# Optimization experiments

Hardware: AMD Instinct MI355X
Metric: run time of the kernel (lower is better)

The kernel has to match this reference:

```python
import jax, jax.numpy as jnp
import numpy as np

N, E, F, H, B = 100000, 3200000, 128, 32, 256
NEG_SLOPE = 0.2  # PyG GATv2Conv default negative_slope


def setup_inputs() -> dict:
    key = jax.random.key(0)
    ks = jax.random.split(key, 8)
    x = jax.random.normal(ks[0], (N, F), jnp.float32)
    edge_index = jax.random.randint(ks[1], (2, E), 0, N, dtype=jnp.int32)
    # sorted graph ids covering all B graphs (PyG batch vector is sorted)
    batch = (jnp.arange(N, dtype=jnp.int32) * B) // N
    init = lambda k, shape, fan: (jax.random.normal(k, shape, jnp.float32) / np.float32(np.sqrt(fan)))
    Wl = init(ks[2], (F, H), F)
    Wr = init(ks[3], (F, H), F)
    att = init(ks[4], (H,), H)
    bias = jnp.zeros((H,), jnp.float32)
    W1 = init(ks[5], (H, 1024), H); b1 = jnp.zeros((1024,), jnp.float32)
    W2 = init(ks[6], (1024, 512), 1024); b2 = jnp.zeros((512,), jnp.float32)
    W3 = init(ks[7], (512, 4), 512); b3 = jnp.zeros((4,), jnp.float32)
    return dict(x=x, edge_index=edge_index, batch=batch, Wl=Wl, Wr=Wr,
                att=att, bias=bias, W1=W1, b1=b1, W2=W2, b2=b2, W3=W3, b3=b3)


def reference(x, edge_index, batch, Wl, Wr, att, bias, W1, b1, W2, b2, W3, b3):
    # ---- GATv2Conv (single head, sum aggregation, self-loops added) ----
    loop = jnp.arange(N, dtype=edge_index.dtype)
    src = jnp.concatenate([edge_index[0], loop])  # [E+N] message sources
    dst = jnp.concatenate([edge_index[1], loop])  # [E+N] message targets
    xl = x @ Wl  # [N,H] source-side transform
    xr = x @ Wr  # [N,H] target-side transform
    # GATv2 score: a^T LeakyReLU(Wl x_src + Wr x_dst)
    e = jax.nn.leaky_relu(xl[src] + xr[dst], NEG_SLOPE) @ att  # [E+N]
    # segment softmax over incoming edges of each target node
    m = jax.ops.segment_max(e, dst, num_segments=N)  # every node has a self-loop
    p = jnp.exp(e - m[dst])
    z = jax.ops.segment_sum(p, dst, num_segments=N)
    alpha = p / z[dst]  # [E+N]
    node_out = jax.ops.segment_sum(alpha[:, None] * xl[src], dst, num_segments=N) + bias  # [N,H]
    # ---- global max pool over each graph ----
    g = jax.ops.segment_max(node_out, batch, num_segments=B)  # [B,H]
    # ---- classification MLP head ----
    h = jax.nn.relu(g @ W1 + b1)
    h = jax.nn.relu(h @ W2 + b2)
    return h @ W3 + b3  # [B,4]
```

## Files before the change

### kernel.cpp

```cpp
#include <hip/hip_runtime.h>
#include <hip/hip_fp16.h>

#define N_NODES 100000
#define N_EDGES 3200000
#define F_IN    128
#define H_DIM   32
#define B_GR    256
#define NEG     0.2f

#define FBIN_SZ  125
#define N_FBIN   (N_NODES / FBIN_SZ)
#define BIN_CAP  5120
#define CPAD     16
#define PART_T   1024
#define EPB_R    8
#define EPB_G    (PART_T * EPB_R)
#define PART_NBLK ((N_EDGES / 4 + EPB_G - 1) / EPB_G)
#define LIN_BLK  ((N_NODES + 63) / 64)

__device__ __forceinline__ unsigned fenc(float f) {
    unsigned u = __float_as_uint(f);
    return (u & 0x80000000u) ? ~u : (u | 0x80000000u);
}
__device__ __forceinline__ float fdec(unsigned u) {
    return (u & 0x80000000u) ? __uint_as_float(u & 0x7FFFFFFFu)
                             : __uint_as_float(~u);
}

__global__ __launch_bounds__(1024) void k_fused(
    const int* __restrict__ ei, int* __restrict__ bcnt, unsigned* __restrict__ binbuf,
    const float* __restrict__ x, const float* __restrict__ Wl,
    const float* __restrict__ Wr, __half* __restrict__ xl16, float* __restrict__ xr)
{
    __shared__ __align__(16) float smem[16384];
    int t = threadIdx.x;

    if (blockIdx.x < PART_NBLK) {
        int* lcnt = (int*)smem;
        int* cur  = lcnt + 1024;
        lcnt[t] = 0;
        __syncthreads();
        int g0 = blockIdx.x * EPB_G;
        const int4* dsrc = (const int4*)(ei + N_EDGES);
        const int4* ssrc = (const int4*)ei;
        #pragma unroll
        for (int r = 0; r < EPB_R; ++r) {
            int i = g0 + r * PART_T + t;
            if (i < N_EDGES / 4) {
                int4 d = dsrc[i];
                atomicAdd(&lcnt[d.x / FBIN_SZ], 1);
                atomicAdd(&lcnt[d.y / FBIN_SZ], 1);
                atomicAdd(&lcnt[d.z / FBIN_SZ], 1);
                atomicAdd(&lcnt[d.w / FBIN_SZ], 1);
            }
        }
        __syncthreads();
        if (t < N_FBIN) {
            int c = lcnt[t];
            if (c > 0) cur[t] = atomicAdd(&bcnt[t * CPAD], c);
        }
        __syncthreads();
        #pragma unroll
        for (int r = 0; r < EPB_R; ++r) {
            int i = g0 + r * PART_T + t;
            if (i < N_EDGES / 4) {
                int4 s = ssrc[i];
                int4 d = dsrc[i];
                int b, p;
                b = d.x / FBIN_SZ; p = atomicAdd(&cur[b], 1);
                binbuf[(size_t)b * BIN_CAP + p] = ((unsigned)(d.x - b * FBIN_SZ) << 17) | (unsigned)s.x;
                b = d.y / FBIN_SZ; p = atomicAdd(&cur[b], 1);
                binbuf[(size_t)b * BIN_CAP + p] = ((unsigned)(d.y - b * FBIN_SZ) << 17) | (unsigned)s.y;
                b = d.z / FBIN_SZ; p = atomicAdd(&cur[b], 1);
                binbuf[(size_t)b * BIN_CAP + p] = ((unsigned)(d.z - b * FBIN_SZ) << 17) | (unsigned)s.z;
                b = d.w / FBIN_SZ; p = atomicAdd(&cur[b], 1);
                binbuf[(size_t)b * BIN_CAP + p] = ((unsigned)(d.w - b * FBIN_SZ) << 17) | (unsigned)s.w;
            }
        }
    } else {
        float* Wls = smem;
        float* Wrs = smem + 4096;
        float* xsb = smem + 8192;
        int blk = blockIdx.x - PART_NBLK;
        for (int i = t; i < F_IN * H_DIM; i += 1024) { Wls[i] = Wl[i]; Wrs[i] = Wr[i]; }
        int q = t >> 8, tq = t & 255;
        size_t base = (size_t)blk * 64 + q * 16;
        bool act = base < N_NODES;
        float* xs = xsb + q * 2048;
        if (act) {
            const float4* xg = (const float4*)(x + base * F_IN);
            float4* xs4 = (float4*)xs;
            xs4[tq] = xg[tq];
            xs4[tq + 256] = xg[tq + 256];
        }
        __syncthreads();
        if (act) {
            int nl = tq >> 5, h = tq & 31;
            float al0 = 0.f, ar0 = 0.f, al1 = 0.f, ar1 = 0.f;
            const float4* xa4 = (const float4*)(xs + nl * F_IN);
            const float4* xb4 = (const float4*)(xs + (nl + 8) * F_IN);
            #pragma unroll 8
            for (int f4 = 0; f4 < 32; ++f4) {
                float4 xa = xa4[f4], xb = xb4[f4];
                int fb = f4 * 4;
                float w;
                w = Wls[(fb + 0) * 32 + h]; al0 = fmaf(xa.x, w, al0); al1 = fmaf(xb.x, w, al1);
                w = Wls[(fb + 1) * 32 + h]; al0 = fmaf(xa.y, w, al0); al1 = fmaf(xb.y, w, al1);
                w = Wls[(fb + 2) * 32 + h]; al0 = fmaf(xa.z, w, al0); al1 = fmaf(xb.z, w, al1);
                w = Wls[(fb + 3) * 32 + h]; al0 = fmaf(xa.w, w, al0); al1 = fmaf(xb.w, w, al1);
                w = Wrs[(fb + 0) * 32 + h]; ar0 = fmaf(xa.x, w, ar0); ar1 = fmaf(xb.x, w, ar1);
                w = Wrs[(fb + 1) * 32 + h]; ar0 = fmaf(xa.y, w, ar0); ar1 = fmaf(xb.y, w, ar1);
                w = Wrs[(fb + 2) * 32 + h]; ar0 = fmaf(xa.z, w, ar0); ar1 = fmaf(xb.z, w, ar1);
                w = Wrs[(fb + 3) * 32 + h]; ar0 = fmaf(xa.w, w, ar0); ar1 = fmaf(xb.w, w, ar1);
            }
            size_t n0 = base + nl, n1 = base + nl + 8;
            xl16[n0 * 32 + h] = __float2half(al0); xr[n0 * 32 + h] = ar0;
            xl16[n1 * 32 + h] = __float2half(al1); xr[n1 * 32 + h] = ar1;
        }
    }
}

__global__ __launch_bounds__(512) void k_aggregate(
    const unsigned* __restrict__ binbuf, const int* __restrict__ bcnt,
    const __half* __restrict__ xl16, const float* __restrict__ xr,
    const float* __restrict__ att, const float* __restrict__ bias,
    const int* __restrict__ batch, unsigned* __restrict__ gu)
{
    __shared__ unsigned eL[BIN_CAP];
    __shared__ int cnt[128];
    __shared__ int sc[128];
    __shared__ int cur[128];
    __shared__ unsigned lmax[64];
    int t = threadIdx.x;
    int bin = blockIdx.x;
    int n_e = bcnt[bin * CPAD];
    const unsigned* bb = binbuf + (size_t)bin * BIN_CAP;

    if (t < 128) cnt[t] = 0;
    if (t < 64) lmax[t] = 0u;
    __syncthreads();
    for (int i = t; i < n_e; i += 512)
        atomicAdd(&cnt[bb[i] >> 17], 1);
    __syncthreads();
    if (t < 128) sc[t] = cnt[t];
    __syncthreads();
    for (int off = 1; off < 128; off <<= 1) {
        int v = 0;
        if (t < 128 && t >= off) v = sc[t - off];
        __syncthreads();
        if (t < 128) sc[t] += v;
        __syncthreads();
    }
    if (t < 128) cur[t] = sc[t] - cnt[t];
    __syncthreads();
    for (int i = t; i < n_e; i += 512) {
        unsigned u = bb[i];
        int p = atomicAdd(&cur[u >> 17], 1);
        eL[p] = u;
    }
    __syncthreads();

    int lane = t & 63;
    int wv = t >> 6;
    int ns = (lane >> 4) & 3;
    int stream = (lane >> 3) & 1;
    int oct = lane & 7;
    const float4 a4 = ((const float4*)att)[oct];
    const float4 b4 = ((const float4*)bias)[oct];
    int lg0 = batch[bin * FBIN_SZ];

    for (int nl = wv * 4 + ns; nl < FBIN_SZ; nl += 32) {
        int n = bin * FBIN_SZ + nl;
        int e0 = (nl > 0) ? sc[nl - 1] : 0;
        int e1 = sc[nl];
        const float4 xr4 = ((const float4*)(xr + (size_t)n * H_DIM))[oct];
        float2 raw = ((const float2*)(xl16 + (size_t)n * H_DIM))[oct];
        float2 sf0 = __half22float2(*(__half2*)&raw.x);
        float2 sf1 = __half22float2(*(__half2*)&raw.y);

        float z = 0.f;
        float4 acc = make_float4(0.f, 0.f, 0.f, 0.f);
        {
            float vx = sf0.x + xr4.x; vx = fmaxf(vx, vx * NEG);
            float vy = sf0.y + xr4.y; vy = fmaxf(vy, vy * NEG);
            float vz = sf1.x + xr4.z; vz = fmaxf(vz, vz * NEG);
            float vw = sf1.y + xr4.w; vw = fmaxf(vw, vw * NEG);
            float pr = vx * a4.x;
            pr = fmaf(vy, a4.y, pr);
            pr = fmaf(vz, a4.z, pr);
            pr = fmaf(vw, a4.w, pr);
            pr += __shfl_xor(pr, 1);
            pr += __shfl_xor(pr, 2);
            pr += __shfl_xor(pr, 4);
            if (stream == 0) {
                float p = __expf(fminf(pr, 70.f));
                z = p;
                acc = make_float4(p * sf0.x, p * sf0.y, p * sf1.x, p * sf1.y);
            }
        }

        int j = e0 + stream;
        for (; j + 2 < e1; j += 4) {
            unsigned uA = eL[j], uB = eL[j + 2];
            int sA = (int)(uA & 0x1FFFFu), sB = (int)(uB & 0x1FFFFu);
            float2 rA = ((const float2*)(xl16 + (size_t)sA * H_DIM))[oct];
            float2 rB = ((const float2*)(xl16 + (size_t)sB * H_DIM))[oct];
            float2 A0 = __half22float2(*(__half2*)&rA.x);
            float2 A1 = __half22float2(*(__half2*)&rA.y);
            float2 B0 = __half22float2(*(__half2*)&rB.x);
            float2 B1 = __half22float2(*(__half2*)&rB.y);
            float pA, pB;
            {
                float vx = A0.x + xr4.x; vx = fmaxf(vx, vx * NEG);
                float vy = A0.y + xr4.y; vy = fmaxf(vy, vy * NEG);
                float vz = A1.x + xr4.z; vz = fmaxf(vz, vz * NEG);
                float vw = A1.y + xr4.w; vw = fmaxf(vw, vw * NEG);
                pA = vx * a4.x; pA = fmaf(vy, a4.y, pA);
                pA = fmaf(vz, a4.z, pA); pA = fmaf(vw, a4.w, pA);
            }
            {
                float vx = B0.x + xr4.x; vx = fmaxf(vx, vx * NEG);
                float vy = B0.y + xr4.y; vy = fmaxf(vy, vy * NEG);
                float vz = B1.x + xr4.z; vz = fmaxf(vz, vz * NEG);
                float vw = B1.y + xr4.w; vw = fmaxf(vw, vw * NEG);
                pB = vx * a4.x; pB = fmaf(vy, a4.y, pB);
                pB = fmaf(vz, a4.z, pB); pB = fmaf(vw, a4.w, pB);
            }
            pA += __shfl_xor(pA, 1); pB += __shfl_xor(pB, 1);
            pA += __shfl_xor(pA, 2); pB += __shfl_xor(pB, 2);
            pA += __shfl_xor(pA, 4); pB += __shfl_xor(pB, 4);
            float eA = __expf(fminf(pA, 70.f));
            float eB = __expf(fminf(pB, 70.f));
            z += eA + eB;
            acc.x = fmaf(eA, A0.x, acc.x); acc.y = fmaf(eA, A0.y, acc.y);
            acc.z = fmaf(eA, A1.x, acc.z); acc.w = fmaf(eA, A1.y, acc.w);
            acc.x = fmaf(eB, B0.x, acc.x); acc.y = fmaf(eB, B0.y, acc.y);
            acc.z = fmaf(eB, B1.x, acc.z); acc.w = fmaf(eB, B1.y, acc.w);
        }
        for (; j < e1; j += 2) {
            unsigned u = eL[j];
            int s = (int)(u & 0x1FFFFu);
            float2 rS = ((const float2*)(xl16 + (size_t)s * H_DIM))[oct];
            float2 S0 = __half22float2(*(__half2*)&rS.x);
            float2 S1 = __half22float2(*(__half2*)&rS.y);
            float vx = S0.x + xr4.x; vx = fmaxf(vx, vx * NEG);
            float vy = S0.y + xr4.y; vy = fmaxf(vy, vy * NEG);
            float vz = S1.x + xr4.z; vz = fmaxf(vz, vz * NEG);
            float vw = S1.y + xr4.w; vw = fmaxf(vw, vw * NEG);
            float pp = vx * a4.x; pp = fmaf(vy, a4.y, pp);
            pp = fmaf(vz, a4.z, pp); pp = fmaf(vw, a4.w, pp);
            pp += __shfl_xor(pp, 1);
            pp += __shfl_xor(pp, 2);
            pp += __shfl_xor(pp, 4);
            float p = __expf(fminf(pp, 70.f));
            z += p;
            acc.x = fmaf(p, S0.x, acc.x); acc.y = fmaf(p, S0.y, acc.y);
            acc.z = fmaf(p, S1.x, acc.z); acc.w = fmaf(p, S1.y, acc.w);
        }

        z += __shfl_xor(z, 8);
        acc.x += __shfl_xor(acc.x, 8);
        acc.y += __shfl_xor(acc.y, 8);
        acc.z += __shfl_xor(acc.z, 8);
        acc.w += __shfl_xor(acc.w, 8);

        if (stream == 0) {
            float inv = 1.f / z;
            int gi = batch[n] - lg0;
            int base = gi * 32 + oct * 4;
            atomicMax(&lmax[base + 0], fenc(fmaf(acc.x, inv, b4.x)));
            atomicMax(&lmax[base + 1], fenc(fmaf(acc.y, inv, b4.y)));
            atomicMax(&lmax[base + 2], fenc(fmaf(acc.z, inv, b4.z)));
            atomicMax(&lmax[base + 3], fenc(fmaf(acc.w, inv, b4.w)));
        }
    }
    __syncthreads();
    if (t < 64) {
        int g = lg0 + (t >> 5);
        int glast = batch[bin * FBIN_SZ + FBIN_SZ - 1];
        if (g <= glast) atomicMax(&gu[g * H_DIM + (t & 31)], lmax[t]);
    }
}

__global__ __launch_bounds__(512) void k_head(
    const unsigned* __restrict__ gu, const float* __restrict__ W1,
    const float* __restrict__ b1, const float* __restrict__ W2,
    const float* __restrict__ b2, const float* __restrict__ W3,
    const float* __restrict__ b3, float* __restrict__ out)
{
    __shared__ float gs[H_DIM];
    __shared__ float h1s[1024];
    __shared__ float h2s[512];
    int b = blockIdx.x, t = threadIdx.x;
    if (t < H_DIM) gs[t] = fdec(gu[b * H_DIM + t]);
    __syncthreads();
    #pragma unroll
    for (int jj = 0; jj < 2; ++jj) {
        int j = jj * 512 + t;
        float a = b1[j];
        #pragma unroll
        for (int k = 0; k < H_DIM; ++k) a = fmaf(gs[k], W1[k * 1024 + j], a);
        h1s[j] = fmaxf(a, 0.f);
    }
    __syncthreads();
    {
        float a0 = 0.f, a1 = 0.f, a2 = 0.f, a3 = 0.f;
        #pragma unroll 4
        for (int k = 0; k < 256; ++k) {
            a0 = fmaf(h1s[k      ], W2[(size_t)(k      ) * 512 + t], a0);
            a1 = fmaf(h1s[k + 256], W2[(size_t)(k + 256) * 512 + t], a1);
            a2 = fmaf(h1s[k + 512], W2[(size_t)(k + 512) * 512 + t], a2);
            a3 = fmaf(h1s[k + 768], W2[(size_t)(k + 768) * 512 + t], a3);
        }
        h2s[t] = fmaxf((a0 + a1) + (a2 + a3) + b2[t], 0.f);
    }
    __syncthreads();
    if (t < 256) {
        int c = t >> 6, lane = t & 63;
        float a = 0.f;
        #pragma unroll
        for (int k = lane; k < 512; k += 64)
            a = fmaf(h2s[k], W3[k * 4 + c], a);
        for (int off = 32; off; off >>= 1) a += __shfl_down(a, off);
        if (lane == 0) out[b * 4 + c] = a + b3[c];
    }
}

extern "C" void kernel_launch(void* const* d_in, const int* in_sizes, int n_in,
                              void* d_out, int out_size, void* d_ws, size_t ws_size,
                              hipStream_t stream)
{
    const float* x     = (const float*)d_in[0];
    const int*   ei    = (const int*)d_in[1];
    const int*   batch = (const int*)d_in[2];
    const float* Wl    = (const float*)d_in[3];
    const float* Wr    = (const float*)d_in[4];
    const float* att   = (const float*)d_in[5];
    const float* bias  = (const float*)d_in[6];
    const float* W1    = (const float*)d_in[7];
    const float* b1    = (const float*)d_in[8];
    const float* W2    = (const float*)d_in[9];
    const float* b2    = (const float*)d_in[10];
    const float* W3    = (const float*)d_in[11];
    const float* b3    = (const float*)d_in[12];
    float* out = (float*)d_out;

    __half*   xl16   = (__half*)d_ws;
    float*    xr     = (float*)(xl16 + (size_t)N_NODES * H_DIM);
    unsigned* binbuf = (unsigned*)(xr + (size_t)N_NODES * H_DIM);
    int*      bcnt   = (int*)(binbuf + (size_t)N_FBIN * BIN_CAP);
    unsigned* gu     = (unsigned*)(bcnt + N_FBIN * CPAD);

    hipMemsetAsync(bcnt, 0, (size_t)(N_FBIN * CPAD + B_GR * H_DIM) * sizeof(int), stream);

    k_fused<<<PART_NBLK + LIN_BLK, 1024, 0, stream>>>(
        ei, bcnt, binbuf, x, Wl, Wr, xl16, xr);
    k_aggregate<<<N_FBIN, 512, 0, stream>>>(binbuf, bcnt, xl16, xr, att, bias, batch, gu);
    k_head<<<B_GR, 512, 0, stream>>>(gu, W1, b1, W2, b2, W3, b3, out);
}
```

Measured before the change: 156.5 us.

## Replace global bin atomics with per-block segmented partition and store xr in fp16

Each partition block now computes a local exclusive scan of its per-bin counts and writes its edges contiguously into its own region, recording per-block segment offsets. This replaces the global atomicAdd on bin counters and the scattered writes into fixed-capacity bins. The aggregate kernel then gathers each bin's edges from all partition blocks' segments, which fragments its reads into many short runs. Separately, xr is stored as fp16 to halve that buffer's traffic, at some cost in precision.

```diff
diff --git a/kernel.cpp b/kernel.cpp
--- a/kernel.cpp
+++ b/kernel.cpp
@@ -11,11 +11,12 @@
 #define FBIN_SZ  125
 #define N_FBIN   (N_NODES / FBIN_SZ)
 #define BIN_CAP  5120
-#define CPAD     16
 #define PART_T   1024
 #define EPB_R    8
 #define EPB_G    (PART_T * EPB_R)
-#define PART_NBLK ((N_EDGES / 4 + EPB_G - 1) / EPB_G)
+#define EPB_E    (EPB_G * 4)
+#define PART_NBLK ((N_EDGES + EPB_E - 1) / EPB_E)
+#define SEG_STRIDE (N_FBIN + 1)
 #define LIN_BLK  ((N_NODES + 63) / 64)
 
 __device__ __forceinline__ unsigned fenc(float f) {
@@ -28,9 +29,9 @@
 }
 
 __global__ __launch_bounds__(1024) void k_fused(
-    const int* __restrict__ ei, int* __restrict__ bcnt, unsigned* __restrict__ binbuf,
+    const int* __restrict__ ei, int* __restrict__ segofs, unsigned* __restrict__ binbuf,
     const float* __restrict__ x, const float* __restrict__ Wl,
-    const float* __restrict__ Wr, __half* __restrict__ xl16, float* __restrict__ xr)
+    const float* __restrict__ Wr, __half* __restrict__ xl16, __half* __restrict__ xr16)
 {
     __shared__ __align__(16) float smem[16384];
     int t = threadIdx.x;
@@ -38,9 +39,11 @@
     if (blockIdx.x < PART_NBLK) {
         int* lcnt = (int*)smem;
         int* cur  = lcnt + 1024;
+        int* wsum = cur + 1024;
+        int blk = blockIdx.x;
         lcnt[t] = 0;
         __syncthreads();
-        int g0 = blockIdx.x * EPB_G;
+        int g0 = blk * EPB_G;
         const int4* dsrc = (const int4*)(ei + N_EDGES);
         const int4* ssrc = (const int4*)ei;
         #pragma unroll
@@ -55,11 +58,27 @@
             }
         }
         __syncthreads();
-        if (t < N_FBIN) {
-            int c = lcnt[t];
-            if (c > 0) cur[t] = atomicAdd(&bcnt[t * CPAD], c);
-        }
-        __syncthreads();
+        int lane = t & 63, w = t >> 6;
+        int v = lcnt[t];
+        int inc = v;
+        #pragma unroll
+        for (int off = 1; off < 64; off <<= 1) {
+            int u2 = __shfl_up(inc, off);
+            if (lane >= off) inc += u2;
+        }
+        if (lane == 63) wsum[w] = inc;
+        __syncthreads();
+        if (t == 0) {
+            int run = 0;
+            #pragma unroll
+            for (int k = 0; k < 16; ++k) { int vv = wsum[k]; wsum[k] = run; run += vv; }
+        }
+        __syncthreads();
+        int excl = inc - v + wsum[w];
+        cur[t] = excl;
+        if (t <= N_FBIN) segofs[(size_t)blk * SEG_STRIDE + t] = excl;
+        __syncthreads();
+        size_t blkbase = (size_t)blk * EPB_E;
         #pragma unroll
         for (int r = 0; r < EPB_R; ++r) {
             int i = g0 + r * PART_T + t;
@@ -68,13 +87,13 @@
                 int4 d = dsrc[i];
                 int b, p;
                 b = d.x / FBIN_SZ; p = atomicAdd(&cur[b], 1);
-                binbuf[(size_t)b * BIN_CAP + p] = ((unsigned)(d.x - b * FBIN_SZ) << 17) | (unsigned)s.x;
+                binbuf[blkbase + p] = ((unsigned)(d.x - b * FBIN_SZ) << 17) | (unsigned)s.x;
                 b = d.y / FBIN_SZ; p = atomicAdd(&cur[b], 1);
-                binbuf[(size_t)b * BIN_CAP + p] = ((unsigned)(d.y - b * FBIN_SZ) << 17) | (unsigned)s.y;
+                binbuf[blkbase + p] = ((unsigned)(d.y - b * FBIN_SZ) << 17) | (unsigned)s.y;
                 b = d.z / FBIN_SZ; p = atomicAdd(&cur[b], 1);
-                binbuf[(size_t)b * BIN_CAP + p] = ((unsigned)(d.z - b * FBIN_SZ) << 17) | (unsigned)s.z;
+                binbuf[blkbase + p] = ((unsigned)(d.z - b * FBIN_SZ) << 17) | (unsigned)s.z;
                 b = d.w / FBIN_SZ; p = atomicAdd(&cur[b], 1);
-                binbuf[(size_t)b * BIN_CAP + p] = ((unsigned)(d.w - b * FBIN_SZ) << 17) | (unsigned)s.w;
+                binbuf[blkbase + p] = ((unsigned)(d.w - b * FBIN_SZ) << 17) | (unsigned)s.w;
             }
         }
     } else {
@@ -114,15 +133,15 @@
                 w = Wrs[(fb + 3) * 32 + h]; ar0 = fmaf(xa.w, w, ar0); ar1 = fmaf(xb.w, w, ar1);
             }
             size_t n0 = base + nl, n1 = base + nl + 8;
-            xl16[n0 * 32 + h] = __float2half(al0); xr[n0 * 32 + h] = ar0;
-            xl16[n1 * 32 + h] = __float2half(al1); xr[n1 * 32 + h] = ar1;
+            xl16[n0 * 32 + h] = __float2half(al0); xr16[n0 * 32 + h] = __float2half(ar0);
+            xl16[n1 * 32 + h] = __float2half(al1); xr16[n1 * 32 + h] = __float2half(ar1);
         }
     }
 }
 
 __global__ __launch_bounds__(512) void k_aggregate(
-    const unsigned* __restrict__ binbuf, const int* __restrict__ bcnt,
-    const __half* __restrict__ xl16, const float* __restrict__ xr,
+    const unsigned* __restrict__ binbuf, const int* __restrict__ segofs,
+    const __half* __restrict__ xl16, const __half* __restrict__ xr16,
     const float* __restrict__ att, const float* __restrict__ bias,
     const int* __restrict__ batch, unsigned* __restrict__ gu)
 {
@@ -130,17 +149,27 @@
     __shared__ int cnt[128];
     __shared__ int sc[128];
     __shared__ int cur[128];
+    __shared__ int llen[PART_NBLK];
+    __shared__ int sbase[PART_NBLK];
     __shared__ unsigned lmax[64];
     int t = threadIdx.x;
     int bin = blockIdx.x;
-    int n_e = bcnt[bin * CPAD];
-    const unsigned* bb = binbuf + (size_t)bin * BIN_CAP;
-
+    int lane = t & 63;
+    int wv = t >> 6;
+
+    if (t < PART_NBLK) {
+        int a = segofs[(size_t)t * SEG_STRIDE + bin];
+        llen[t]  = segofs[(size_t)t * SEG_STRIDE + bin + 1] - a;
+        sbase[t] = t * EPB_E + a;
+    }
     if (t < 128) cnt[t] = 0;
     if (t < 64) lmax[t] = 0u;
     __syncthreads();
-    for (int i = t; i < n_e; i += 512)
-        atomicAdd(&cnt[bb[i] >> 17], 1);
+    for (int k = wv; k < PART_NBLK; k += 8) {
+        int gb = sbase[k], L = llen[k];
+        for (int i = lane; i < L; i += 64)
+            atomicAdd(&cnt[binbuf[gb + i] >> 17], 1);
+    }
     __syncthreads();
     if (t < 128) sc[t] = cnt[t];
     __syncthreads();
@@ -153,15 +182,16 @@
     }
     if (t < 128) cur[t] = sc[t] - cnt[t];
     __syncthreads();
-    for (int i = t; i < n_e; i += 512) {
-        unsigned u = bb[i];
-        int p = atomicAdd(&cur[u >> 17], 1);
-        eL[p] = u;
-    }
-    __syncthreads();
-
-    int lane = t & 63;
-    int wv = t >> 6;
+    for (int k = wv; k < PART_NBLK; k += 8) {
+        int gb = sbase[k], L = llen[k];
+        for (int i = lane; i < L; i += 64) {
+            unsigned u = binbuf[gb + i];
+            int p = atomicAdd(&cur[u >> 17], 1);
+            eL[p] = u;
+        }
+    }
+    __syncthreads();
+
     int ns = (lane >> 4) & 3;
     int stream = (lane >> 3) & 1;
     int oct = lane & 7;
@@ -173,7 +203,9 @@
         int n = bin * FBIN_SZ + nl;
         int e0 = (nl > 0) ? sc[nl - 1] : 0;
         int e1 = sc[nl];
-        const float4 xr4 = ((const float4*)(xr + (size_t)n * H_DIM))[oct];
+        float2 rawr = ((const float2*)(xr16 + (size_t)n * H_DIM))[oct];
+        float2 xr0 = __half22float2(*(__half2*)&rawr.x);
+        float2 xr1 = __half22float2(*(__half2*)&rawr.y);
         float2 raw = ((const float2*)(xl16 + (size_t)n * H_DIM))[oct];
         float2 sf0 = __half22float2(*(__half2*)&raw.x);
         float2 sf1 = __half22float2(*(__half2*)&raw.y);
@@ -181,10 +213,10 @@
         float z = 0.f;
         float4 acc = make_float4(0.f, 0.f, 0.f, 0.f);
         {
-            float vx = sf0.x + xr4.x; vx = fmaxf(vx, vx * NEG);
-            float vy = sf0.y + xr4.y; vy = fmaxf(vy, vy * NEG);
-            float vz = sf1.x + xr4.z; vz = fmaxf(vz, vz * NEG);
-            float vw = sf1.y + xr4.w; vw = fmaxf(vw, vw * NEG);
+            float vx = sf0.x + xr0.x; vx = fmaxf(vx, vx * NEG);
+            float vy = sf0.y + xr0.y; vy = fmaxf(vy, vy * NEG);
+            float vz = sf1.x + xr1.x; vz = fmaxf(vz, vz * NEG);
+            float vw = sf1.y + xr1.y; vw = fmaxf(vw, vw * NEG);
             float pr = vx * a4.x;
             pr = fmaf(vy, a4.y, pr);
             pr = fmaf(vz, a4.z, pr);
@@ -211,18 +243,18 @@
             float2 B1 = __half22float2(*(__half2*)&rB.y);
             float pA, pB;
             {
-                float vx = A0.x + xr4.x; vx = fmaxf(vx, vx * NEG);
-                float vy = A0.y + xr4.y; vy = fmaxf(vy, vy * NEG);
-                float vz = A1.x + xr4.z; vz = fmaxf(vz, vz * NEG);
-                float vw = A1.y + xr4.w; vw = fmaxf(vw, vw * NEG);
+                float vx = A0.x + xr0.x; vx = fmaxf(vx, vx * NEG);
+                float vy = A0.y + xr0.y; vy = fmaxf(vy, vy * NEG);
+                float vz = A1.x + xr1.x; vz = fmaxf(vz, vz * NEG);
+                float vw = A1.y + xr1.y; vw = fmaxf(vw, vw * NEG);
                 pA = vx * a4.x; pA = fmaf(vy, a4.y, pA);
                 pA = fmaf(vz, a4.z, pA); pA = fmaf(vw, a4.w, pA);
             }
             {
-                float vx = B0.x + xr4.x; vx = fmaxf(vx, vx * NEG);
-                float vy = B0.y + xr4.y; vy = fmaxf(vy, vy * NEG);
-                float vz = B1.x + xr4.z; vz = fmaxf(vz, vz * NEG);
-                float vw = B1.y + xr4.w; vw = fmaxf(vw, vw * NEG);
+                float vx = B0.x + xr0.x; vx = fmaxf(vx, vx * NEG);
+                float vy = B0.y + xr0.y; vy = fmaxf(vy, vy * NEG);
+                float vz = B1.x + xr1.x; vz = fmaxf(vz, vz * NEG);
+                float vw = B1.y + xr1.y; vw = fmaxf(vw, vw * NEG);
                 pB = vx * a4.x; pB = fmaf(vy, a4.y, pB);
                 pB = fmaf(vz, a4.z, pB); pB = fmaf(vw, a4.w, pB);
             }
@@ -243,10 +275,10 @@
             float2 rS = ((const float2*)(xl16 + (size_t)s * H_DIM))[oct];
             float2 S0 = __half22float2(*(__half2*)&rS.x);
             float2 S1 = __half22float2(*(__half2*)&rS.y);
-            float vx = S0.x + xr4.x; vx = fmaxf(vx, vx * NEG);
-            float vy = S0.y + xr4.y; vy = fmaxf(vy, vy * NEG);
-            float vz = S1.x + xr4.z; vz = fmaxf(vz, vz * NEG);
-            float vw = S1.y + xr4.w; vw = fmaxf(vw, vw * NEG);
+            float vx = S0.x + xr0.x; vx = fmaxf(vx, vx * NEG);
+            float vy = S0.y + xr0.y; vy = fmaxf(vy, vy * NEG);
+            float vz = S1.x + xr1.x; vz = fmaxf(vz, vz * NEG);
+            float vw = S1.y + xr1.y; vw = fmaxf(vw, vw * NEG);
             float pp = vx * a4.x; pp = fmaf(vy, a4.y, pp);
             pp = fmaf(vz, a4.z, pp); pp = fmaf(vw, a4.w, pp);
             pp += __shfl_xor(pp, 1);
@@ -346,15 +378,15 @@
     float* out = (float*)d_out;
 
     __half*   xl16   = (__half*)d_ws;
-    float*    xr     = (float*)(xl16 + (size_t)N_NODES * H_DIM);
-    unsigned* binbuf = (unsigned*)(xr + (size_t)N_NODES * H_DIM);
-    int*      bcnt   = (int*)(binbuf + (size_t)N_FBIN * BIN_CAP);
-    unsigned* gu     = (unsigned*)(bcnt + N_FBIN * CPAD);
-
-    hipMemsetAsync(bcnt, 0, (size_t)(N_FBIN * CPAD + B_GR * H_DIM) * sizeof(int), stream);
+    __half*   xr16   = xl16 + (size_t)N_NODES * H_DIM;
+    unsigned* binbuf = (unsigned*)(xr16 + (size_t)N_NODES * H_DIM);
+    int*      segofs = (int*)(binbuf + (size_t)PART_NBLK * EPB_E);
+    unsigned* gu     = (unsigned*)(segofs + (size_t)PART_NBLK * SEG_STRIDE);
+
+    hipMemsetAsync(gu, 0, (size_t)B_GR * H_DIM * sizeof(int), stream);
 
     k_fused<<<PART_NBLK + LIN_BLK, 1024, 0, stream>>>(
-        ei, bcnt, binbuf, x, Wl, Wr, xl16, xr);
-    k_aggregate<<<N_FBIN, 512, 0, stream>>>(binbuf, bcnt, xl16, xr, att, bias, batch, gu);
+        ei, segofs, binbuf, x, Wl, Wr, xl16, xr16);
+    k_aggregate<<<N_FBIN, 512, 0, stream>>>(binbuf, segofs, xl16, xr16, att, bias, batch, gu);
     k_head<<<B_GR, 512, 0, stream>>>(gu, W1, b1, W2, b2, W3, b3, out);
 }
```

Result: slower. 165.2 us (+5.5%).
